# Kernel tuning notes

Measured on AMD Instinct MI355X. Metric: run time of the kernel, lower is better.

The kernel has to match this reference:

```python
import jax, jax.numpy as jnp
import numpy as np
from jax import lax

IN_F = 512   # encoder output dim
MEL = 80     # mel bins (memory_dim)
R = 7        # reduction factor
ATT = 128    # attention dim
B = 64
T_ENC = 512
T_MEL = 700  # must be divisible by R -> 100 decoder steps


def _gru(x, h, w_ih, w_hh, b_ih, b_hh):
    # torch.nn.GRUCell math
    gi = x @ w_ih.T + b_ih
    gh = h @ w_hh.T + b_hh
    ir, iz, inn = jnp.split(gi, 3, axis=-1)
    hr, hz, hn = jnp.split(gh, 3, axis=-1)
    r = jax.nn.sigmoid(ir + hr)
    z = jax.nn.sigmoid(iz + hz)
    return (1.0 - z) * jnp.tanh(inn + r * hn) + z * h


_PARAM_SHAPES = {
    'prenet_w1': (256, MEL), 'prenet_b1': (256,),
    'prenet_w2': (128, 256), 'prenet_b2': (128,),
    'attrnn_w_ih': (768, IN_F + 128), 'attrnn_w_hh': (768, 256),
    'attrnn_b_ih': (768,), 'attrnn_b_hh': (768,),
    'q_w': (ATT, 256), 'inp_w': (ATT, IN_F), 'v_w': (1, ATT), 'v_b': (1,),
    'loc_conv': (32, 2, 31), 'loc_w': (ATT, 32),
    'pd_w': (256, 256 + IN_F), 'pd_b': (256,),
    'dec1_w_ih': (768, 256), 'dec1_w_hh': (768, 256), 'dec1_b_ih': (768,), 'dec1_b_hh': (768,),
    'dec2_w_ih': (768, 256), 'dec2_w_hh': (768, 256), 'dec2_b_ih': (768,), 'dec2_b_hh': (768,),
    'mel_w': (MEL * R, 256), 'mel_b': (MEL * R,),
    'stop_w': (1, 256 + MEL * R), 'stop_b': (1,),
}


def setup_inputs() -> dict:
    key = jax.random.key(0)
    ks = iter(jax.random.split(key, 40))
    d = {
        'inputs': jax.random.normal(next(ks), (B, T_ENC, IN_F), jnp.float32),
        'memory': jax.random.normal(next(ks), (B, T_MEL, MEL), jnp.float32),
        'mask': jnp.ones((B, T_ENC), dtype=bool),
    }
    for n, s in _PARAM_SHAPES.items():
        d[n] = jax.random.normal(next(ks), s, jnp.float32) * 0.02
    return d


def reference(inputs, memory, mask, prenet_w1, prenet_b1, prenet_w2, prenet_b2,
              attrnn_w_ih, attrnn_w_hh, attrnn_b_ih, attrnn_b_hh,
              q_w, inp_w, v_w, v_b, loc_conv, loc_w, pd_w, pd_b,
              dec1_w_ih, dec1_w_hh, dec1_b_ih, dec1_b_hh,
              dec2_w_ih, dec2_w_hh, dec2_b_ih, dec2_b_hh,
              mel_w, mel_b, stop_w, stop_b):
    Bq, T_enc, _ = inputs.shape
    # attention.preprocess_inputs: [B, T_enc, ATT], computed once
    proc_in = jnp.einsum('btd,ad->bta', inputs, inp_w)
    # _reshape_memory: [B, T_mel, MEL] -> [T_steps, B, R*MEL]
    mem = memory.reshape(Bq, -1, R * MEL).transpose(1, 0, 2)
    # teacher forcing: step 0 uses zero memory_input, step t uses frame t-1
    xs = jnp.concatenate([jnp.zeros_like(mem[:1]), mem[:-1]], axis=0)

    def step(carry, x):
        h_att, h1, h2, ctx, aw, awc = carry
        # memory_size<=0 path: keep last mel frame of previous group
        m_in = x[:, MEL * (R - 1):]
        # prenet (original, dropout disabled)
        p = jax.nn.relu(m_in @ prenet_w1.T + prenet_b1)
        p = jax.nn.relu(p @ prenet_w2.T + prenet_b2)
        # attention RNN
        h_att = _gru(jnp.concatenate([p, ctx], axis=-1), h_att,
                     attrnn_w_ih, attrnn_w_hh, attrnn_b_ih, attrnn_b_hh)
        # location-sensitive attention
        pq = h_att @ q_w.T                              # [B, ATT]
        loc = jnp.stack([aw, awc], axis=1)              # [B, 2, T_enc]
        pl = lax.conv_general_dilated(loc, loc_conv, (1,), [(15, 15)],
                                      dimension_numbers=('NCH', 'OIH', 'NCH'))
        pl = jnp.einsum('bct,ac->bta', pl, loc_w)       # [B, T_enc, ATT]
        e = (jnp.tanh(pq[:, None, :] + proc_in + pl) @ v_w.T)[..., 0] + v_b
        e = jnp.where(mask, e, -1e9)
        align = jax.nn.softmax(e, axis=-1)              # [B, T_enc]
        ctx = jnp.einsum('bt,btd->bd', align, inputs)   # [B, IN_F]
        awc = awc + align
        # decoder RNNs with residual connections
        dec = jnp.concatenate([h_att, ctx], axis=-1) @ pd_w.T + pd_b
        h1 = _gru(dec, h1, dec1_w_ih, dec1_w_hh, dec1_b_ih, dec1_b_hh)
        dec = h1 + dec
        h2 = _gru(dec, h2, dec2_w_ih, dec2_w_hh, dec2_b_ih, dec2_b_hh)
        dec = h2 + dec
        out = dec @ mel_w.T + mel_b                     # [B, R*MEL]
        # separate_stopnet=True: stopnet input is detached
        sin = lax.stop_gradient(jnp.concatenate([dec, out], axis=-1))
        stop = (sin @ stop_w.T + stop_b)[:, 0]
        return (h_att, h1, h2, ctx, align, awc), (out, align, stop)

    z = lambda n: jnp.zeros((Bq, n), inputs.dtype)
    zt = jnp.zeros((Bq, T_enc), inputs.dtype)
    carry0 = (z(256), z(256), z(256), z(IN_F), zt, zt)
    _, (outs, atts, stops) = lax.scan(step, carry0, xs)
    # _parse_outputs
    outputs = outs.transpose(1, 0, 2).reshape(Bq, -1, MEL).transpose(0, 2, 1)  # [B, MEL, T_mel]
    return outputs, atts.transpose(1, 0, 2), stops.T
```

## Files before the change

### kernel.cpp

```cpp
#include <hip/hip_runtime.h>
#include <hip/hip_bf16.h>


typedef unsigned int u32;

#ifndef __has_builtin
#define __has_builtin(x) 0
#endif

#define NSTEP 100

#define PK_ATTIH 0
#define PK_ATTHH 245760
#define PK_Q     344064
#define PK_PD    360448
#define PK_D1IH  458752
#define PK_D1HH  557056
#define PK_D2IH  655360
#define PK_D2HH  753664
#define PK_MEL   851968
#define W1T_U    923648
#define W2T_U    944128
#define PROCF_U  976896
#define P2ALL_U  3074048

#define OUT_ATT  3584000
#define OUT_STOP 6860800

typedef _Float16 h2 __attribute__((ext_vector_type(2)));
union U4 { uint4 v; _Float16 h[8]; };

__device__ __forceinline__ float fastrcp(float x) { return __builtin_amdgcn_rcpf(x); }
__device__ __forceinline__ float sig_p(float x) { return 1.f / (1.f + __expf(-x)); }
__device__ __forceinline__ float tanh_f(float x) {
    x = fminf(fmaxf(x, -15.f), 15.f);
    float e2 = __expf(2.f * x);
    return (e2 - 1.f) * fastrcp(e2 + 1.f);
}

__device__ __forceinline__ float dot2(u32 w, u32 x, float acc) {
    h2 wh = __builtin_bit_cast(h2, w);
    h2 xh = __builtin_bit_cast(h2, x);
#if __has_builtin(__builtin_amdgcn_fdot2)
    return __builtin_amdgcn_fdot2(wh, xh, acc, false);
#else
    return acc + (float)wh.x * (float)xh.x + (float)wh.y * (float)xh.y;
#endif
}

__device__ __forceinline__ u32 packh2(float a, float b) {
    h2 h; h.x = (_Float16)a; h.y = (_Float16)b;
    return __builtin_bit_cast(u32, h);
}

__global__ void tkern(const float* __restrict__ src, float* __restrict__ dst, int O, int K) {
    int i = blockIdx.x * blockDim.x + threadIdx.x;
    if (i < O * K) {
        int o = i % O, k = i / O;
        dst[i] = src[o * K + k];
    }
}

__global__ void packw(const float* __restrict__ src, u32* __restrict__ dst, int O, int K) {
    int i = blockIdx.x * blockDim.x + threadIdx.x;
    int n = O * (K >> 1);
    if (i < n) {
        int o = i % O, p = i / O;
        dst[i] = packh2(src[o * K + 2 * p], src[o * K + 2 * p + 1]);
    }
}

__global__ void prenet_kern(const float* __restrict__ memory,
                            const float* __restrict__ w1T, const float* __restrict__ b1,
                            const float* __restrict__ w2T, const float* __restrict__ b2,
                            float* __restrict__ p2all) {
    __shared__ float mi[80];
    __shared__ float p1[256];
    int blk = blockIdx.x;
    int t = blk >> 6, b = blk & 63;
    int tid = threadIdx.x;
    if (tid < 80) mi[tid] = (t == 0) ? 0.f : memory[(b * 700 + (7 * t - 1)) * 80 + tid];
    __syncthreads();
    float acc = b1[tid];
#pragma unroll 4
    for (int k = 0; k < 80; k++) acc += mi[k] * w1T[k * 256 + tid];
    p1[tid] = fmaxf(acc, 0.f);
    __syncthreads();
    if (tid < 128) {
        float a2 = b2[tid];
#pragma unroll 4
        for (int k = 0; k < 256; k++) a2 += p1[k] * w2T[k * 128 + tid];
        p2all[(t * 64 + b) * 128 + tid] = fmaxf(a2, 0.f);
    }
}

__global__ void proc_kern(const float* __restrict__ inputs, const float* __restrict__ inpT,
                          _Float16* __restrict__ procF) {
    __shared__ float xin[8][512];
    int blk = blockIdx.x;
    int b = blk >> 6, t0 = (blk & 63) << 3;
    int tid = threadIdx.x;
    for (int i = tid; i < 8 * 512; i += 1024)
        xin[i >> 9][i & 511] = inputs[((size_t)b * 512 + t0 + (i >> 9)) * 512 + (i & 511)];
    __syncthreads();
    int r = tid >> 7, a = tid & 127;
    float acc = 0.f;
#pragma unroll 4
    for (int d = 0; d < 512; d++) acc += xin[r][d] * inpT[d * 128 + a];
    procF[((size_t)(b * 512) + t0 + r) * 128 + a] = (_Float16)acc;
}

__launch_bounds__(1024, 1)
__global__ void decoder_kern(const float* __restrict__ inputs,
                             const u32* __restrict__ wsu,
                             const float* __restrict__ att_b_ih, const float* __restrict__ att_b_hh,
                             const float* __restrict__ v_w, const float* __restrict__ v_b,
                             const float* __restrict__ lcg, const float* __restrict__ lwg,
                             const float* __restrict__ pd_b,
                             const float* __restrict__ d1b_ih, const float* __restrict__ d1b_hh,
                             const float* __restrict__ d2b_ih, const float* __restrict__ d2b_hh,
                             const float* __restrict__ mel_b,
                             const float* __restrict__ stop_w, const float* __restrict__ stop_b,
                             float* __restrict__ out) {
    const int b = blockIdx.x;
    const int tid = threadIdx.x;

    const uint4* w_attih = (const uint4*)(wsu + PK_ATTIH);
    const uint4* w_atthh = (const uint4*)(wsu + PK_ATTHH);
    const uint4* w_q     = (const uint4*)(wsu + PK_Q);
    const uint4* w_pd    = (const uint4*)(wsu + PK_PD);
    const uint4* w_d1ih  = (const uint4*)(wsu + PK_D1IH);
    const uint4* w_d1hh  = (const uint4*)(wsu + PK_D1HH);
    const uint4* w_d2ih  = (const uint4*)(wsu + PK_D2IH);
    const uint4* w_d2hh  = (const uint4*)(wsu + PK_D2HH);
    const uint4* w_mel   = (const uint4*)(wsu + PK_MEL);
    const _Float16* procF = (const _Float16*)(wsu + PROCF_U);
    const float* p2all   = (const float*)(wsu + P2ALL_U);

    __shared__ float h_att[256], h1[256], h2[256], dec[256];
    __shared__ float awp[542], awcp[542];
    __shared__ float pq[128], ebuf[512], red[32], mout[560];
    __shared__ float convbuf[32 * 513];
    __shared__ __align__(16) float scrA[4096];
    __shared__ __align__(16) float scrB[3072];
    __shared__ u32 xpatt[320];
    __shared__ u32 xppd[384];
    __shared__ u32 decp[128], h1p[128], h2p[128];

    for (int i = tid; i < 256; i += 1024) { h_att[i] = 0.f; h1[i] = 0.f; h2[i] = 0.f; dec[i] = 0.f; }
    for (int i = tid; i < 542; i += 1024) { awp[i] = 0.f; awcp[i] = 0.f; }
    for (int i = tid; i < 320; i += 1024) xpatt[i] = 0u;
    for (int i = tid; i < 384; i += 1024) xppd[i] = 0u;
    if (tid < 128) { decp[tid] = 0u; h1p[tid] = 0u; h2p[tid] = 0u; }
    if (tid >= 960) {
        int j = tid - 960;
        xpatt[j] = packh2(p2all[(size_t)b * 128 + 2 * j], p2all[(size_t)b * 128 + 2 * j + 1]);
    }
    const float vb0 = v_b[0];
    const float sb0 = stop_b[0];
    __syncthreads();

    for (int step = 0; step < NSTEP; step++) {
        if (tid < 768) {
            const int og = tid % 192;
            const int ks = tid / 192;
            float4 ai = {0.f, 0.f, 0.f, 0.f};
            float4 ah4 = {0.f, 0.f, 0.f, 0.f};
#pragma unroll 8
            for (int p = ks * 80; p < ks * 80 + 80; p++) {
                uint4 w = w_attih[p * 192 + og];
                u32 x = xpatt[p];
                ai.x = dot2(w.x, x, ai.x); ai.y = dot2(w.y, x, ai.y);
                ai.z = dot2(w.z, x, ai.z); ai.w = dot2(w.w, x, ai.w);
            }
#pragma unroll 8
            for (int p = ks * 32; p < ks * 32 + 32; p++) {
                uint4 w = w_atthh[p * 192 + og];
                u32 x = xppd[p];
                ah4.x = dot2(w.x, x, ah4.x); ah4.y = dot2(w.y, x, ah4.y);
                ah4.z = dot2(w.z, x, ah4.z); ah4.w = dot2(w.w, x, ah4.w);
            }
            *(float4*)&scrA[ks * 768 + og * 4] = ai;
            *(float4*)&scrB[ks * 768 + og * 4] = ah4;
        }
        __syncthreads();

        if (tid < 128) {
            float hv[2];
#pragma unroll
            for (int j = 0; j < 2; j++) {
                const int o = tid * 2 + j;
                float gr = att_b_ih[o], gz = att_b_ih[256 + o], gn = att_b_ih[512 + o];
                float hr = att_b_hh[o], hz = att_b_hh[256 + o], hn = att_b_hh[512 + o];
#pragma unroll
                for (int s = 0; s < 4; s++) {
                    gr += scrA[s * 768 + o]; gz += scrA[s * 768 + 256 + o]; gn += scrA[s * 768 + 512 + o];
                    hr += scrB[s * 768 + o]; hz += scrB[s * 768 + 256 + o]; hn += scrB[s * 768 + 512 + o];
                }
                float r = sig_p(gr + hr), z = sig_p(gz + hz);
                float n = tanhf(gn + r * hn);
                hv[j] = (1.f - z) * n + z * h_att[o];
                h_att[o] = hv[j];
            }
            xppd[tid] = packh2(hv[0], hv[1]);
        }
        __syncthreads();

        if (tid < 128) {
            const int og = tid & 31, ks = tid >> 5;
            float4 acc = {0.f, 0.f, 0.f, 0.f};
#pragma unroll 8
            for (int p = ks * 32; p < ks * 32 + 32; p++) {
                uint4 w = w_q[p * 32 + og];
                u32 x = xppd[p];
                acc.x = dot2(w.x, x, acc.x); acc.y = dot2(w.y, x, acc.y);
                acc.z = dot2(w.z, x, acc.z); acc.w = dot2(w.w, x, acc.w);
            }
            *(float4*)&scrA[ks * 128 + og * 4] = acc;
        } else if (tid >= 512) {
            const int tp = tid - 512;
            float cr[32];
#pragma unroll
            for (int c = 0; c < 32; c++) cr[c] = 0.f;
            for (int k = 0; k < 31; k++) {
                float a1 = awp[tp + k], a2 = awcp[tp + k];
#pragma unroll
                for (int c = 0; c < 32; c++)
                    cr[c] += lcg[c * 62 + k] * a1 + lcg[c * 62 + 31 + k] * a2;
            }
#pragma unroll
            for (int c = 0; c < 32; c++) convbuf[c * 513 + tp] = cr[c];
        }
        __syncthreads();

        if (tid < 128) {
            pq[tid] = scrA[tid] + scrA[128 + tid] + scrA[256 + tid] + scrA[384 + tid];
        }
        __syncthreads();

        {
            const int tp = tid & 511;
            const int ah = tid >> 9;
            const int a0 = ah * 64;
            float cr2[32];
#pragma unroll
            for (int c = 0; c < 32; c++) cr2[c] = convbuf[c * 513 + tp];
            const uint4* pf4 = (const uint4*)(procF + ((size_t)(b * 512 + tp)) * 128 + a0);
            float acc = 0.f;
            for (int l = 0; l < 8; l++) {
                U4 u; u.v = pf4[l];
#pragma unroll
                for (int j = 0; j < 8; j++) {
                    const int a = l * 8 + j;
                    float s = pq[a0 + a] + (float)u.h[j];
#pragma unroll
                    for (int c = 0; c < 32; c++) s += lwg[(a0 + a) * 32 + c] * cr2[c];
                    acc += v_w[a0 + a] * tanh_f(s);
                }
            }
            scrB[tid] = acc;
        }
        __syncthreads();

        float e_reg = -1e30f;
        if (tid < 512) e_reg = scrB[tid] + scrB[512 + tid] + vb0;
        {
            float v = e_reg;
#pragma unroll
            for (int off = 32; off; off >>= 1) v = fmaxf(v, __shfl_down(v, off, 64));
            if (tid < 512 && (tid & 63) == 0) red[tid >> 6] = v;
        }
        __syncthreads();
        if (tid == 0) {
            float m = red[0];
            for (int w = 1; w < 8; w++) m = fmaxf(m, red[w]);
            red[16] = m;
        }
        __syncthreads();
        float ex = 0.f;
        if (tid < 512) ex = __expf(e_reg - red[16]);
        {
            float v = ex;
#pragma unroll
            for (int off = 32; off; off >>= 1) v += __shfl_down(v, off, 64);
            if (tid < 512 && (tid & 63) == 0) red[tid >> 6] = v;
        }
        __syncthreads();
        if (tid == 0) {
            float s = 0.f;
            for (int w = 0; w < 8; w++) s += red[w];
            red[17] = s;
        }
        __syncthreads();
        if (tid < 512) {
            float al = ex * fastrcp(red[17]);
            ebuf[tid] = al;
            awp[15 + tid] = al;
            awcp[15 + tid] += al;
            out[OUT_ATT + ((size_t)b * 100 + step) * 512 + tid] = al;
        }
        __syncthreads();

        {
            const int dg = tid & 127, ts = tid >> 7;
            const float4* ib = (const float4*)(inputs + ((size_t)b * 512 + ts * 64) * 512);
            float4 acc = {0.f, 0.f, 0.f, 0.f};
#pragma unroll 8
            for (int t = 0; t < 64; t++) {
                float al = ebuf[ts * 64 + t];
                float4 xv = ib[(size_t)t * 128 + dg];
                acc.x += al * xv.x; acc.y += al * xv.y; acc.z += al * xv.z; acc.w += al * xv.w;
            }
            *(float4*)&scrA[ts * 512 + dg * 4] = acc;
        }
        __syncthreads();

        if (tid < 256) {
            float s0 = 0.f, s1 = 0.f;
#pragma unroll
            for (int q = 0; q < 8; q++) { s0 += scrA[q * 512 + 2 * tid]; s1 += scrA[q * 512 + 2 * tid + 1]; }
            u32 pr = packh2(s0, s1);
            xpatt[64 + tid] = pr;
            xppd[128 + tid] = pr;
        }
        __syncthreads();

        {
            const int og = tid & 63, ks = tid >> 6;
            float4 acc = {0.f, 0.f, 0.f, 0.f};
#pragma unroll 8
            for (int p = ks * 24; p < ks * 24 + 24; p++) {
                uint4 w = w_pd[p * 64 + og];
                u32 x = xppd[p];
                acc.x = dot2(w.x, x, acc.x); acc.y = dot2(w.y, x, acc.y);
                acc.z = dot2(w.z, x, acc.z); acc.w = dot2(w.w, x, acc.w);
            }
            *(float4*)&scrA[ks * 256 + og * 4] = acc;
        }
        __syncthreads();

        if (tid < 128) {
            float d0 = pd_b[2 * tid], d1 = pd_b[2 * tid + 1];
#pragma unroll
            for (int q = 0; q < 16; q++) { d0 += scrA[q * 256 + 2 * tid]; d1 += scrA[q * 256 + 2 * tid + 1]; }
            dec[2 * tid] = d0; dec[2 * tid + 1] = d1;
            decp[tid] = packh2(d0, d1);
        }
        __syncthreads();

        if (tid < 768) {
            const int og = tid % 192;
            const int ks = tid / 192;
            float4 ai = {0.f, 0.f, 0.f, 0.f};
            float4 ah4 = {0.f, 0.f, 0.f, 0.f};
#pragma unroll 8
            for (int p = ks * 32; p < ks * 32 + 32; p++) {
                uint4 w1 = w_d1ih[p * 192 + og];
                uint4 w2 = w_d1hh[p * 192 + og];
                u32 xd = decp[p], xh = h1p[p];
                ai.x = dot2(w1.x, xd, ai.x); ai.y = dot2(w1.y, xd, ai.y);
                ai.z = dot2(w1.z, xd, ai.z); ai.w = dot2(w1.w, xd, ai.w);
                ah4.x = dot2(w2.x, xh, ah4.x); ah4.y = dot2(w2.y, xh, ah4.y);
                ah4.z = dot2(w2.z, xh, ah4.z); ah4.w = dot2(w2.w, xh, ah4.w);
            }
            *(float4*)&scrA[ks * 768 + og * 4] = ai;
            *(float4*)&scrB[ks * 768 + og * 4] = ah4;
        }
        __syncthreads();

        if (tid < 128) {
            float hv[2], dv[2];
#pragma unroll
            for (int j = 0; j < 2; j++) {
                const int o = tid * 2 + j;
                float gr = d1b_ih[o], gz = d1b_ih[256 + o], gn = d1b_ih[512 + o];
                float hr = d1b_hh[o], hz = d1b_hh[256 + o], hn = d1b_hh[512 + o];
#pragma unroll
                for (int s = 0; s < 4; s++) {
                    gr += scrA[s * 768 + o]; gz += scrA[s * 768 + 256 + o]; gn += scrA[s * 768 + 512 + o];
                    hr += scrB[s * 768 + o]; hz += scrB[s * 768 + 256 + o]; hn += scrB[s * 768 + 512 + o];
                }
                float r = sig_p(gr + hr), z = sig_p(gz + hz);
                float n = tanhf(gn + r * hn);
                hv[j] = (1.f - z) * n + z * h1[o];
                h1[o] = hv[j];
                dv[j] = hv[j] + dec[o];
                dec[o] = dv[j];
            }
            h1p[tid] = packh2(hv[0], hv[1]);
            decp[tid] = packh2(dv[0], dv[1]);
        }
        __syncthreads();

        if (tid < 768) {
            const int og = tid % 192;
            const int ks = tid / 192;
            float4 ai = {0.f, 0.f, 0.f, 0.f};
            float4 ah4 = {0.f, 0.f, 0.f, 0.f};
#pragma unroll 8
            for (int p = ks * 32; p < ks * 32 + 32; p++) {
                uint4 w1 = w_d2ih[p * 192 + og];
                uint4 w2 = w_d2hh[p * 192 + og];
                u32 xd = decp[p], xh = h2p[p];
                ai.x = dot2(w1.x, xd, ai.x); ai.y = dot2(w1.y, xd, ai.y);
                ai.z = dot2(w1.z, xd, ai.z); ai.w = dot2(w1.w, xd, ai.w);
                ah4.x = dot2(w2.x, xh, ah4.x); ah4.y = dot2(w2.y, xh, ah4.y);
                ah4.z = dot2(w2.z, xh, ah4.z); ah4.w = dot2(w2.w, xh, ah4.w);
            }
            *(float4*)&scrA[ks * 768 + og * 4] = ai;
            *(float4*)&scrB[ks * 768 + og * 4] = ah4;
        }
        __syncthreads();

        if (tid < 128) {
            float hv[2], dv[2];
#pragma unroll
            for (int j = 0; j < 2; j++) {
                const int o = tid * 2 + j;
                float gr = d2b_ih[o], gz = d2b_ih[256 + o], gn = d2b_ih[512 + o];
                float hr = d2b_hh[o], hz = d2b_hh[256 + o], hn = d2b_hh[512 + o];
#pragma unroll
                for (int s = 0; s < 4; s++) {
                    gr += scrA[s * 768 + o]; gz += scrA[s * 768 + 256 + o]; gn += scrA[s * 768 + 512 + o];
                    hr += scrB[s * 768 + o]; hz += scrB[s * 768 + 256 + o]; hn += scrB[s * 768 + 512 + o];
                }
                float r = sig_p(gr + hr), z = sig_p(gz + hz);
                float n = tanhf(gn + r * hn);
                hv[j] = (1.f - z) * n + z * h2[o];
                h2[o] = hv[j];
                dv[j] = hv[j] + dec[o];
                dec[o] = dv[j];
            }
            h2p[tid] = packh2(hv[0], hv[1]);
            decp[tid] = packh2(dv[0], dv[1]);
        }
        __syncthreads();

        if (tid < 560) {
            const int og = tid % 140;
            const int ks = tid / 140;
            float4 acc = {0.f, 0.f, 0.f, 0.f};
#pragma unroll 8
            for (int p = ks * 32; p < ks * 32 + 32; p++) {
                uint4 w = w_mel[p * 140 + og];
                u32 x = decp[p];
                acc.x = dot2(w.x, x, acc.x); acc.y = dot2(w.y, x, acc.y);
                acc.z = dot2(w.z, x, acc.z); acc.w = dot2(w.w, x, acc.w);
            }
            *(float4*)&scrA[ks * 560 + og * 4] = acc;
        }
        __syncthreads();

        if (tid < 280) {
#pragma unroll
            for (int j = 0; j < 2; j++) {
                const int o = 2 * tid + j;
                float m = mel_b[o];
#pragma unroll
                for (int s = 0; s < 4; s++) m += scrA[s * 560 + o];
                mout[o] = m;
                int mm = o % 80, jj = o / 80;
                out[((size_t)b * 80 + mm) * 700 + 7 * step + jj] = m;
            }
        }
        __syncthreads();

        {
            float v = 0.f;
            if (tid < 816) v = ((tid < 256) ? dec[tid] : mout[tid - 256]) * stop_w[tid];
            if (tid < 832) {
#pragma unroll
                for (int off = 32; off; off >>= 1) v += __shfl_down(v, off, 64);
                if ((tid & 63) == 0) red[tid >> 6] = v;
            }
            if (tid >= 960 && step + 1 < NSTEP) {
                int j = tid - 960;
                const float* p2n = p2all + ((size_t)(step + 1) * 64 + b) * 128;
                xpatt[j] = packh2(p2n[2 * j], p2n[2 * j + 1]);
            }
        }
        __syncthreads();
        if (tid == 0) {
            float s = sb0;
            for (int w = 0; w < 13; w++) s += red[w];
            out[OUT_STOP + (size_t)b * 100 + step] = s;
        }
        __syncthreads();
    }
}

extern "C" void kernel_launch(void* const* d_in, const int* in_sizes, int n_in,
                              void* d_out, int out_size, void* d_ws, size_t ws_size,
                              hipStream_t stream) {
    const float* inputs    = (const float*)d_in[0];
    const float* memory    = (const float*)d_in[1];
    const float* prenet_w1 = (const float*)d_in[3];
    const float* prenet_b1 = (const float*)d_in[4];
    const float* prenet_w2 = (const float*)d_in[5];
    const float* prenet_b2 = (const float*)d_in[6];
    const float* att_w_ih  = (const float*)d_in[7];
    const float* att_w_hh  = (const float*)d_in[8];
    const float* att_b_ih  = (const float*)d_in[9];
    const float* att_b_hh  = (const float*)d_in[10];
    const float* q_w       = (const float*)d_in[11];
    const float* inp_w     = (const float*)d_in[12];
    const float* v_w       = (const float*)d_in[13];
    const float* v_b       = (const float*)d_in[14];
    const float* loc_conv  = (const float*)d_in[15];
    const float* loc_w     = (const float*)d_in[16];
    const float* pd_w      = (const float*)d_in[17];
    const float* pd_b      = (const float*)d_in[18];
    const float* d1_w_ih   = (const float*)d_in[19];
    const float* d1_w_hh   = (const float*)d_in[20];
    const float* d1_b_ih   = (const float*)d_in[21];
    const float* d1_b_hh   = (const float*)d_in[22];
    const float* d2_w_ih   = (const float*)d_in[23];
    const float* d2_w_hh   = (const float*)d_in[24];
    const float* d2_b_ih   = (const float*)d_in[25];
    const float* d2_b_hh   = (const float*)d_in[26];
    const float* mel_w     = (const float*)d_in[27];
    const float* mel_b     = (const float*)d_in[28];
    const float* stop_w    = (const float*)d_in[29];
    const float* stop_b    = (const float*)d_in[30];

    u32* wsu = (u32*)d_ws;
    float* out = (float*)d_out;

    auto P = [&](const float* src, int off, int O, int K) {
        int n = O * (K / 2);
        packw<<<(n + 255) / 256, 256, 0, stream>>>(src, wsu + off, O, K);
    };
    P(att_w_ih, PK_ATTIH, 768, 640);
    P(att_w_hh, PK_ATTHH, 768, 256);
    P(q_w,      PK_Q,     128, 256);
    P(pd_w,     PK_PD,    256, 768);
    P(d1_w_ih,  PK_D1IH,  768, 256);
    P(d1_w_hh,  PK_D1HH,  768, 256);
    P(d2_w_ih,  PK_D2IH,  768, 256);
    P(d2_w_hh,  PK_D2HH,  768, 256);
    P(mel_w,    PK_MEL,   560, 256);

    tkern<<<(256 * 80 + 255) / 256, 256, 0, stream>>>(prenet_w1, (float*)(wsu + W1T_U), 256, 80);
    tkern<<<(128 * 256 + 255) / 256, 256, 0, stream>>>(prenet_w2, (float*)(wsu + W2T_U), 128, 256);

    prenet_kern<<<6400, 256, 0, stream>>>(memory, (float*)(wsu + W1T_U), prenet_b1,
                                          (float*)(wsu + W2T_U), prenet_b2,
                                          (float*)(wsu + P2ALL_U));

    {
        float* inpT = (float*)(wsu + P2ALL_U + 819200);
        tkern<<<(128 * 512 + 255) / 256, 256, 0, stream>>>(inp_w, inpT, 128, 512);
        proc_kern<<<4096, 1024, 0, stream>>>(inputs, inpT, (_Float16*)(wsu + PROCF_U));
    }

    decoder_kern<<<64, 1024, 0, stream>>>(inputs, wsu,
                                          att_b_ih, att_b_hh, v_w, v_b,
                                          loc_conv, loc_w, pd_b,
                                          d1_b_ih, d1_b_hh, d2_b_ih, d2_b_hh,
                                          mel_b, stop_w, stop_b, out);
}
```

Measured before the change: 17.61 ms.

## Stage location weights in LDS, fp16 dot2 energy, fewer barriers, nontemporal loads

The decoder kernel now stages the location-layer weights (packed to fp16), the transposed location conv weights, v_w and stop_w in shared memory, so they are no longer read from global memory on every step. The location-energy inner product uses fp16 dot2 instead of fp32 FMAs, and the q projection is computed directly by one thread per output, which removes a reduction pass and a barrier. Softmax max and sum are now reduced redundantly by every thread rather than by thread 0 behind extra barriers, and the trailing barrier is dropped. It also adds nontemporal loads for streamed data, swaps tanhf for the fast tanh in the GRUs and raises launch_bounds occupancy to 4, which costs precision in the energy term and may lead to register spills.

After: 15.48 ms. 12.1% less time.

```diff
diff --git a/kernel.cpp b/kernel.cpp
--- a/kernel.cpp
+++ b/kernel.cpp
@@ -28,6 +28,8 @@
 #define OUT_STOP 6860800
 
 typedef _Float16 h2 __attribute__((ext_vector_type(2)));
+typedef float f32x4 __attribute__((ext_vector_type(4)));
+typedef unsigned int u32x4 __attribute__((ext_vector_type(4)));
 union U4 { uint4 v; _Float16 h[8]; };
 
 __device__ __forceinline__ float fastrcp(float x) { return __builtin_amdgcn_rcpf(x); }
@@ -51,6 +53,18 @@
 __device__ __forceinline__ u32 packh2(float a, float b) {
     h2 h; h.x = (_Float16)a; h.y = (_Float16)b;
     return __builtin_bit_cast(u32, h);
+}
+
+__device__ __forceinline__ float4 ntload_f4(const float* p) {
+    f32x4 v = __builtin_nontemporal_load((const f32x4*)p);
+    float4 r; r.x = v.x; r.y = v.y; r.z = v.z; r.w = v.w; return r;
+}
+__device__ __forceinline__ uint4 ntload_u4(const uint4* p) {
+    u32x4 v = __builtin_nontemporal_load((const u32x4*)p);
+    uint4 r; r.x = v.x; r.y = v.y; r.z = v.z; r.w = v.w; return r;
+}
+__device__ __forceinline__ float ntload_f(const float* p) {
+    return __builtin_nontemporal_load(p);
 }
 
 __global__ void tkern(const float* __restrict__ src, float* __restrict__ dst, int O, int K) {
@@ -110,7 +124,7 @@
     procF[((size_t)(b * 512) + t0 + r) * 128 + a] = (_Float16)acc;
 }
 
-__launch_bounds__(1024, 1)
+__launch_bounds__(1024, 4)
 __global__ void decoder_kern(const float* __restrict__ inputs,
                              const u32* __restrict__ wsu,
                              const float* __restrict__ att_b_ih, const float* __restrict__ att_b_hh,
@@ -127,7 +141,6 @@
 
     const uint4* w_attih = (const uint4*)(wsu + PK_ATTIH);
     const uint4* w_atthh = (const uint4*)(wsu + PK_ATTHH);
-    const uint4* w_q     = (const uint4*)(wsu + PK_Q);
     const uint4* w_pd    = (const uint4*)(wsu + PK_PD);
     const uint4* w_d1ih  = (const uint4*)(wsu + PK_D1IH);
     const uint4* w_d1hh  = (const uint4*)(wsu + PK_D1HH);
@@ -146,12 +159,24 @@
     __shared__ u32 xpatt[320];
     __shared__ u32 xppd[384];
     __shared__ u32 decp[128], h1p[128], h2p[128];
+    __shared__ __align__(16) u32 lwp_lds[128 * 16];
+    __shared__ __align__(16) float lcgT[62 * 32];
+    __shared__ float vws[128];
+    __shared__ float stopws[816];
 
     for (int i = tid; i < 256; i += 1024) { h_att[i] = 0.f; h1[i] = 0.f; h2[i] = 0.f; dec[i] = 0.f; }
     for (int i = tid; i < 542; i += 1024) { awp[i] = 0.f; awcp[i] = 0.f; }
     for (int i = tid; i < 320; i += 1024) xpatt[i] = 0u;
     for (int i = tid; i < 384; i += 1024) xppd[i] = 0u;
     if (tid < 128) { decp[tid] = 0u; h1p[tid] = 0u; h2p[tid] = 0u; }
+    for (int i = tid; i < 2048; i += 1024)
+        lwp_lds[i] = packh2(lwg[2 * i], lwg[2 * i + 1]);
+    for (int i = tid; i < 62 * 32; i += 1024) {
+        int k = i >> 5, c = i & 31;
+        lcgT[i] = lcg[c * 62 + k];
+    }
+    if (tid < 128) vws[tid] = v_w[tid];
+    if (tid < 816) stopws[tid] = stop_w[tid];
     if (tid >= 960) {
         int j = tid - 960;
         xpatt[j] = packh2(p2all[(size_t)b * 128 + 2 * j], p2all[(size_t)b * 128 + 2 * j + 1]);
@@ -198,7 +223,7 @@
                     hr += scrB[s * 768 + o]; hz += scrB[s * 768 + 256 + o]; hn += scrB[s * 768 + 512 + o];
                 }
                 float r = sig_p(gr + hr), z = sig_p(gz + hz);
-                float n = tanhf(gn + r * hn);
+                float n = tanh_f(gn + r * hn);
                 hv[j] = (1.f - z) * n + z * h_att[o];
                 h_att[o] = hv[j];
             }
@@ -207,55 +232,63 @@
         __syncthreads();
 
         if (tid < 128) {
-            const int og = tid & 31, ks = tid >> 5;
-            float4 acc = {0.f, 0.f, 0.f, 0.f};
-#pragma unroll 8
-            for (int p = ks * 32; p < ks * 32 + 32; p++) {
-                uint4 w = w_q[p * 32 + og];
-                u32 x = xppd[p];
-                acc.x = dot2(w.x, x, acc.x); acc.y = dot2(w.y, x, acc.y);
-                acc.z = dot2(w.z, x, acc.z); acc.w = dot2(w.w, x, acc.w);
-            }
-            *(float4*)&scrA[ks * 128 + og * 4] = acc;
+            const u32* wqu = wsu + PK_Q;
+            float qa = 0.f;
+#pragma unroll 8
+            for (int p = 0; p < 128; p++) qa = dot2(wqu[p * 128 + tid], xppd[p], qa);
+            pq[tid] = qa;
         } else if (tid >= 512) {
             const int tp = tid - 512;
             float cr[32];
 #pragma unroll
             for (int c = 0; c < 32; c++) cr[c] = 0.f;
+#pragma clang loop unroll_count(2)
             for (int k = 0; k < 31; k++) {
                 float a1 = awp[tp + k], a2 = awcp[tp + k];
-#pragma unroll
-                for (int c = 0; c < 32; c++)
-                    cr[c] += lcg[c * 62 + k] * a1 + lcg[c * 62 + 31 + k] * a2;
+                const float4* l1 = (const float4*)&lcgT[k * 32];
+                const float4* l2 = (const float4*)&lcgT[(31 + k) * 32];
+#pragma unroll
+                for (int cc = 0; cc < 8; cc++) {
+                    float4 w1 = l1[cc], w2 = l2[cc];
+                    cr[4 * cc]     += w1.x * a1 + w2.x * a2;
+                    cr[4 * cc + 1] += w1.y * a1 + w2.y * a2;
+                    cr[4 * cc + 2] += w1.z * a1 + w2.z * a2;
+                    cr[4 * cc + 3] += w1.w * a1 + w2.w * a2;
+                }
             }
 #pragma unroll
             for (int c = 0; c < 32; c++) convbuf[c * 513 + tp] = cr[c];
-        }
-        __syncthreads();
-
-        if (tid < 128) {
-            pq[tid] = scrA[tid] + scrA[128 + tid] + scrA[256 + tid] + scrA[384 + tid];
         }
         __syncthreads();
 
         {
             const int tp = tid & 511;
-            const int ah = tid >> 9;
-            const int a0 = ah * 64;
+            const int a0 = (tid >> 9) << 6;
             float cr2[32];
 #pragma unroll
             for (int c = 0; c < 32; c++) cr2[c] = convbuf[c * 513 + tp];
+            u32 cr2p[16];
+#pragma unroll
+            for (int cp = 0; cp < 16; cp++) cr2p[cp] = packh2(cr2[2 * cp], cr2[2 * cp + 1]);
             const uint4* pf4 = (const uint4*)(procF + ((size_t)(b * 512 + tp)) * 128 + a0);
             float acc = 0.f;
+#pragma clang loop unroll_count(2)
             for (int l = 0; l < 8; l++) {
-                U4 u; u.v = pf4[l];
+                U4 u; u.v = ntload_u4(pf4 + l);
 #pragma unroll
                 for (int j = 0; j < 8; j++) {
                     const int a = l * 8 + j;
                     float s = pq[a0 + a] + (float)u.h[j];
-#pragma unroll
-                    for (int c = 0; c < 32; c++) s += lwg[(a0 + a) * 32 + c] * cr2[c];
-                    acc += v_w[a0 + a] * tanh_f(s);
+                    const uint4* lw = (const uint4*)&lwp_lds[(a0 + a) * 16];
+#pragma unroll
+                    for (int q = 0; q < 4; q++) {
+                        uint4 w = lw[q];
+                        s = dot2(w.x, cr2p[4 * q], s);
+                        s = dot2(w.y, cr2p[4 * q + 1], s);
+                        s = dot2(w.z, cr2p[4 * q + 2], s);
+                        s = dot2(w.w, cr2p[4 * q + 3], s);
+                    }
+                    acc += vws[a0 + a] * tanh_f(s);
                 }
             }
             scrB[tid] = acc;
@@ -271,29 +304,21 @@
             if (tid < 512 && (tid & 63) == 0) red[tid >> 6] = v;
         }
         __syncthreads();
-        if (tid == 0) {
-            float m = red[0];
-            for (int w = 1; w < 8; w++) m = fmaxf(m, red[w]);
-            red[16] = m;
-        }
-        __syncthreads();
+        float smax = fmaxf(fmaxf(fmaxf(red[0], red[1]), fmaxf(red[2], red[3])),
+                           fmaxf(fmaxf(red[4], red[5]), fmaxf(red[6], red[7])));
         float ex = 0.f;
-        if (tid < 512) ex = __expf(e_reg - red[16]);
+        if (tid < 512) ex = __expf(e_reg - smax);
         {
             float v = ex;
 #pragma unroll
             for (int off = 32; off; off >>= 1) v += __shfl_down(v, off, 64);
-            if (tid < 512 && (tid & 63) == 0) red[tid >> 6] = v;
-        }
-        __syncthreads();
-        if (tid == 0) {
-            float s = 0.f;
-            for (int w = 0; w < 8; w++) s += red[w];
-            red[17] = s;
+            if (tid < 512 && (tid & 63) == 0) red[8 + (tid >> 6)] = v;
         }
         __syncthreads();
         if (tid < 512) {
-            float al = ex * fastrcp(red[17]);
+            float ssum = ((red[8] + red[9]) + (red[10] + red[11])) +
+                         ((red[12] + red[13]) + (red[14] + red[15]));
+            float al = ex * fastrcp(ssum);
             ebuf[tid] = al;
             awp[15 + tid] = al;
             awcp[15 + tid] += al;
@@ -303,12 +328,12 @@
 
         {
             const int dg = tid & 127, ts = tid >> 7;
-            const float4* ib = (const float4*)(inputs + ((size_t)b * 512 + ts * 64) * 512);
+            const float* ib = inputs + ((size_t)b * 512 + ts * 64) * 512;
             float4 acc = {0.f, 0.f, 0.f, 0.f};
 #pragma unroll 8
             for (int t = 0; t < 64; t++) {
                 float al = ebuf[ts * 64 + t];
-                float4 xv = ib[(size_t)t * 128 + dg];
+                float4 xv = ntload_f4(ib + (size_t)t * 512 + dg * 4);
                 acc.x += al * xv.x; acc.y += al * xv.y; acc.z += al * xv.z; acc.w += al * xv.w;
             }
             *(float4*)&scrA[ts * 512 + dg * 4] = acc;
@@ -381,7 +406,7 @@
                     hr += scrB[s * 768 + o]; hz += scrB[s * 768 + 256 + o]; hn += scrB[s * 768 + 512 + o];
                 }
                 float r = sig_p(gr + hr), z = sig_p(gz + hz);
-                float n = tanhf(gn + r * hn);
+                float n = tanh_f(gn + r * hn);
                 hv[j] = (1.f - z) * n + z * h1[o];
                 h1[o] = hv[j];
                 dv[j] = hv[j] + dec[o];
@@ -425,7 +450,7 @@
                     hr += scrB[s * 768 + o]; hz += scrB[s * 768 + 256 + o]; hn += scrB[s * 768 + 512 + o];
                 }
                 float r = sig_p(gr + hr), z = sig_p(gz + hz);
-                float n = tanhf(gn + r * hn);
+                float n = tanh_f(gn + r * hn);
                 hv[j] = (1.f - z) * n + z * h2[o];
                 h2[o] = hv[j];
                 dv[j] = hv[j] + dec[o];
@@ -467,7 +492,7 @@
 
         {
             float v = 0.f;
-            if (tid < 816) v = ((tid < 256) ? dec[tid] : mout[tid - 256]) * stop_w[tid];
+            if (tid < 816) v = ((tid < 256) ? dec[tid] : mout[tid - 256]) * stopws[tid];
             if (tid < 832) {
 #pragma unroll
                 for (int off = 32; off; off >>= 1) v += __shfl_down(v, off, 64);
@@ -476,7 +501,7 @@
             if (tid >= 960 && step + 1 < NSTEP) {
                 int j = tid - 960;
                 const float* p2n = p2all + ((size_t)(step + 1) * 64 + b) * 128;
-                xpatt[j] = packh2(p2n[2 * j], p2n[2 * j + 1]);
+                xpatt[j] = packh2(ntload_f(p2n + 2 * j), ntload_f(p2n + 2 * j + 1));
             }
         }
         __syncthreads();
@@ -485,7 +510,6 @@
             for (int w = 0; w < 13; w++) s += red[w];
             out[OUT_STOP + (size_t)b * 100 + step] = s;
         }
-        __syncthreads();
     }
 }
 
```
